# Optimization experiments

Measured on AMD Instinct MI355X. Metric: run time of the kernel, lower is better.

## Reference

```python
import jax, jax.numpy as jnp
import numpy as np

N_NODES = 100000
N_EDGES = 1600000
D_FEAT = 128
HIDDEN = 256
N_CLASSES = 40


def setup_inputs() -> dict:
    key = jax.random.key(0)
    ks = jax.random.split(key, 6)
    x = jax.random.normal(ks[0], (N_NODES, D_FEAT), dtype=jnp.float32)
    edge_index = jax.random.randint(ks[1], (2, N_EDGES), 0, N_NODES, dtype=jnp.int32)
    # Glorot-ish scaled weights
    w1_l = jax.random.normal(ks[2], (HIDDEN, D_FEAT), dtype=jnp.float32) / np.sqrt(D_FEAT)
    w1_r = jax.random.normal(ks[3], (HIDDEN, D_FEAT), dtype=jnp.float32) / np.sqrt(D_FEAT)
    w2_l = jax.random.normal(ks[4], (N_CLASSES, HIDDEN), dtype=jnp.float32) / np.sqrt(HIDDEN)
    w2_r = jax.random.normal(ks[5], (N_CLASSES, HIDDEN), dtype=jnp.float32) / np.sqrt(HIDDEN)
    b1_l = jnp.zeros((HIDDEN,), jnp.float32)
    b2_l = jnp.zeros((N_CLASSES,), jnp.float32)
    return {"x": x, "edge_index": edge_index, "w1_l": w1_l, "b1_l": b1_l,
            "w1_r": w1_r, "w2_l": w2_l, "b2_l": b2_l, "w2_r": w2_r}


def _sage_conv(x, src, dst, n_nodes, w_l, b_l, w_r):
    # mean aggregation of source-node features onto target nodes
    msg = x[src]                                                  # [E, d]
    agg = jax.ops.segment_sum(msg, dst, num_segments=n_nodes)     # [N, d]
    cnt = jax.ops.segment_sum(jnp.ones((dst.shape[0], 1), x.dtype), dst,
                              num_segments=n_nodes)               # [N, 1]
    agg = agg / jnp.maximum(cnt, 1.0)
    # out = lin_l(agg) + lin_r(x); lin_l has bias, lin_r does not (PyG default)
    return agg @ w_l.T + b_l + x @ w_r.T


def reference(x, edge_index, w1_l, b1_l, w1_r, w2_l, b2_l, w2_r):
    n_nodes = x.shape[0]
    src, dst = edge_index[0], edge_index[1]
    h = jax.nn.relu(_sage_conv(x, src, dst, n_nodes, w1_l, b1_l, w1_r))
    # dropout is identity in eval mode
    out = _sage_conv(h, src, dst, n_nodes, w2_l, b2_l, w2_r)
    return jax.nn.log_softmax(out, axis=1)
```

## Files before the change

### kernel.cpp

```cpp
#include <hip/hip_runtime.h>
#include <hip/hip_bf16.h>
#include <stdint.h>

#define NN 100000
#define NE 1600000
#define DF 128
#define DH 256
#define NC 40
#define BSHIFT 8
#define NBKT 391
#define EPB 8192
#define NBIN_BLOCKS ((NE + EPB - 1) / EPB)
#define BKT_SLACK 2048

typedef __attribute__((ext_vector_type(8))) short short8;
typedef __attribute__((ext_vector_type(4))) float f32x4;

typedef const __attribute__((address_space(1))) unsigned int* gas1;
typedef __attribute__((address_space(3))) unsigned int* las3;

__device__ __forceinline__ void gload16(const void* g, void* l) {
  __builtin_amdgcn_global_load_lds((gas1)g, (las3)l, 16, 0, 0);
}

__device__ __forceinline__ unsigned short f2bf(float f) {
  union { float f; unsigned u; } v; v.f = f;
  unsigned r = v.u + 0x7FFFu + ((v.u >> 16) & 1u);
  return (unsigned short)(r >> 16);
}
__device__ __forceinline__ float bflo(unsigned u) {
  union { unsigned u; float f; } v; v.u = u << 16; return v.f;
}
__device__ __forceinline__ float bfhi(unsigned u) {
  union { unsigned u; float f; } v; v.u = u & 0xFFFF0000u; return v.f;
}

__global__ void k_xbf16(const float* __restrict__ x, unsigned* __restrict__ xb) {
  int i = blockIdx.x * blockDim.x + threadIdx.x;
  if (i < (NN + 1) * 64) {
    unsigned pk = 0u;
    if (i < NN * 64) {
      float2 v = ((const float2*)x)[i];
      pk = ((unsigned)f2bf(v.y) << 16) | f2bf(v.x);
    }
    xb[i] = pk;
  }
}

__global__ __launch_bounds__(256) void k_bhist(const int* __restrict__ dst, int* __restrict__ bcnt) {
  __shared__ int h[NBKT];
  int tid = threadIdx.x;
  for (int b = tid; b < NBKT; b += 256) h[b] = 0;
  __syncthreads();
  int base = blockIdx.x * EPB;
  int n = NE - base; if (n > EPB) n = EPB;
  for (int i = tid; i < n; i += 256) atomicAdd(&h[dst[base + i] >> BSHIFT], 1);
  __syncthreads();
  for (int b = tid; b < NBKT; b += 256) if (h[b]) atomicAdd(&bcnt[b], h[b]);
}

__global__ __launch_bounds__(512) void k_bscan(const int* __restrict__ bcnt,
                                               int* __restrict__ boff, int* __restrict__ bcur,
                                               unsigned short* __restrict__ Pb) {
  __shared__ int s[512];
  int tid = threadIdx.x;
  int v = (tid < NBKT) ? bcnt[tid] : 0;
  s[tid] = v;
  __syncthreads();
  for (int off = 1; off < 512; off <<= 1) {
    int a = (tid >= off) ? s[tid - off] : 0;
    __syncthreads();
    s[tid] += a;
    __syncthreads();
  }
  int excl = s[tid] - v;
  if (tid < NBKT) { boff[tid] = excl; bcur[tid] = excl; }
  if (tid == NBKT) boff[NBKT] = excl;
  if (tid >= 448 && tid < 480) ((unsigned*)(Pb + (size_t)NN * 64))[tid - 448] = 0u;
}

__global__ __launch_bounds__(256) void k_bin(const int* __restrict__ src, const int* __restrict__ dst,
                                             int* __restrict__ bcur, unsigned* __restrict__ pairs) {
  __shared__ int hcnt[NBKT];
  __shared__ int hbase[NBKT];
  int tid = threadIdx.x;
  for (int b = tid; b < NBKT; b += 256) hcnt[b] = 0;
  __syncthreads();
  int base = blockIdx.x * EPB;
  int n = NE - base; if (n > EPB) n = EPB;
  for (int i = tid; i < n; i += 256) atomicAdd(&hcnt[dst[base + i] >> BSHIFT], 1);
  __syncthreads();
  for (int b = tid; b < NBKT; b += 256) hbase[b] = hcnt[b] ? atomicAdd(&bcur[b], hcnt[b]) : 0;
  __syncthreads();
  for (int b = tid; b < NBKT; b += 256) hcnt[b] = 0;
  __syncthreads();
  for (int i = tid; i < n; i += 256) {
    int s = src[base + i], d = dst[base + i];
    int b = d >> BSHIFT;
    int slot = atomicAdd(&hcnt[b], 1);
    pairs[hbase[b] + slot] = (unsigned)s | ((unsigned)(d & 255) << 17);
  }
}

__global__ __launch_bounds__(256) void k_csr(const unsigned* __restrict__ pairs,
                                             const int* __restrict__ boff,
                                             int* __restrict__ deg, int* __restrict__ row_ptr8,
                                             int* __restrict__ csr8) {
  __shared__ int ncnt[256];
  __shared__ int noff[256];
  int tid = threadIdx.x;
  int b = blockIdx.x;
  int base = boff[b], end = boff[b + 1];
  int base8 = base + BKT_SLACK * b;
  ncnt[tid] = 0;
  __syncthreads();
  for (int e = base + tid; e < end; e += 256) atomicAdd(&ncnt[pairs[e] >> 17], 1);
  __syncthreads();
  int cnt = ncnt[tid];
  int pcnt = (cnt + 7) & ~7;
  noff[tid] = pcnt;
  __syncthreads();
  for (int off = 1; off < 256; off <<= 1) {
    int a = (tid >= off) ? noff[tid - off] : 0;
    __syncthreads();
    noff[tid] += a;
    __syncthreads();
  }
  int pexcl = noff[tid] - pcnt;
  __syncthreads();
  noff[tid] = pexcl;
  ncnt[tid] = 0;
  __syncthreads();
  int gnode = (b << BSHIFT) + tid;
  if (gnode < NN) { deg[gnode] = cnt; row_ptr8[gnode] = base8 + pexcl; }
  for (int e = base + tid; e < end; e += 256) {
    unsigned p = pairs[e];
    int ld = p >> 17;
    int slot = atomicAdd(&ncnt[ld], 1);
    csr8[base8 + noff[ld] + slot] = (int)(p & 0x1FFFFu);
  }
  for (int k = cnt; k < pcnt; ++k) csr8[base8 + pexcl + k] = NN;
}

__global__ void k_packw(const float* __restrict__ w1l, const float* __restrict__ w1r,
                        const float* __restrict__ w2l, const float* __restrict__ w2r,
                        unsigned short* __restrict__ Wc, unsigned short* __restrict__ W2c) {
  int i = blockIdx.x * blockDim.x + threadIdx.x;
  if (i < 256 * 256) {
    int o = i >> 8, k = i & 255;
    float v = (k < 128) ? w1l[o * 128 + k] : w1r[o * 128 + (k - 128)];
    Wc[i] = f2bf(v);
  }
  int j = i - 256 * 256;
  if (j >= 0 && j < 80 * 256) {
    int o = j >> 8, k = j & 255;
    float v = (o < 40) ? w2l[o * 256 + k] : w2r[(o - 40) * 256 + k];
    W2c[j] = f2bf(v);
  }
}

__global__ void k_agg1(const unsigned* __restrict__ xb, const int* __restrict__ row_ptr8,
                       const int* __restrict__ deg, const int* __restrict__ csr8,
                       unsigned* __restrict__ A1) {
  int w = threadIdx.x >> 6, lane = threadIdx.x & 63;
  int node = blockIdx.x * 4 + w;
  if (node >= NN) return;
  int dg = deg[node];
  int rs = row_ptr8[node];
  int pdeg = (dg + 7) & ~7;
  int half = lane >> 5, li = lane & 31;
  float a0 = 0.f, a1 = 0.f, a2 = 0.f, a3 = 0.f;
  const unsigned* xp = xb + li * 2;
  for (int e = rs; e < rs + pdeg; e += 8) {
#pragma unroll
    for (int j = 0; j < 4; ++j) {
      int idx = csr8[e + 2 * j + half];
      uint2 v = *(const uint2*)(xp + (size_t)idx * 64);
      a0 += bflo(v.x); a1 += bfhi(v.x);
      a2 += bflo(v.y); a3 += bfhi(v.y);
    }
  }
  a0 += __shfl_xor(a0, 32);
  a1 += __shfl_xor(a1, 32);
  a2 += __shfl_xor(a2, 32);
  a3 += __shfl_xor(a3, 32);
  if (half == 0) {
    float inv = 1.f / (float)(dg > 0 ? dg : 1);
    uint2 pk;
    pk.x = ((unsigned)f2bf(a1 * inv) << 16) | f2bf(a0 * inv);
    pk.y = ((unsigned)f2bf(a3 * inv) << 16) | f2bf(a2 * inv);
    *(uint2*)(A1 + (size_t)node * 64 + li * 2) = pk;
  }
}

__global__ __launch_bounds__(256) void k_fused(const unsigned short* __restrict__ A1,
                                               const unsigned short* __restrict__ XB,
                                               const unsigned short* __restrict__ Wc,
                                               const float* __restrict__ b1,
                                               const unsigned short* __restrict__ W2c,
                                               unsigned short* __restrict__ Pb,
                                               float* __restrict__ R) {
  __shared__ __align__(16) unsigned short sA[64 * 64];
  __shared__ __align__(16) unsigned short sB[256 * 64];
  __shared__ __align__(16) unsigned short sH[64 * 256];
  int tid = threadIdx.x;
  int w = tid >> 6, lane = tid & 63;
  int brow = blockIdx.x * 64;
  int wr = (w >> 1) * 32, wc = (w & 1) * 128;
  f32x4 acc[2][8] = {};

  for (int kt = 0; kt < 4; ++kt) {
    const unsigned short* srcA = (kt < 2) ? A1 : XB;
    int kcol = (kt & 1) * 64;
#pragma unroll
    for (int t = 0; t < 2; ++t) {
      int c = t * 256 + tid;
      int r = c >> 3, cc = c & 7;
      int scc = cc ^ (r & 7);
      int gr = brow + r; if (gr > NN - 1) gr = NN - 1;
      gload16(srcA + (size_t)gr * 128 + kcol + scc * 8, sA + c * 8);
    }
#pragma unroll
    for (int t = 0; t < 8; ++t) {
      int c = t * 256 + tid;
      int r = c >> 3, cc = c & 7;
      int scc = cc ^ (r & 7);
      gload16(Wc + (size_t)r * 256 + kt * 64 + scc * 8, sB + c * 8);
    }
    __syncthreads();
#pragma unroll
    for (int kg = 0; kg < 2; ++kg) {
      short8 af[2], bfr[8];
#pragma unroll
      for (int m = 0; m < 2; ++m) {
        int row = wr + m * 16 + (lane & 15);
        int cch = (kg * 4 + (lane >> 4)) ^ (row & 7);
        af[m] = *(const short8*)(sA + row * 64 + cch * 8);
      }
#pragma unroll
      for (int n = 0; n < 8; ++n) {
        int row = wc + n * 16 + (lane & 15);
        int cch = (kg * 4 + (lane >> 4)) ^ (row & 7);
        bfr[n] = *(const short8*)(sB + row * 64 + cch * 8);
      }
#pragma unroll
      for (int m = 0; m < 2; ++m)
#pragma unroll
        for (int n = 0; n < 8; ++n)
          acc[m][n] = __builtin_amdgcn_mfma_f32_16x16x32_bf16(af[m], bfr[n], acc[m][n], 0, 0, 0);
    }
    __syncthreads();
  }

  {
    int colbase = wc + (lane & 15);
    int rowb = wr + (lane >> 4) * 4;
#pragma unroll
    for (int n = 0; n < 8; ++n) {
      int col = colbase + n * 16;
      float bias = b1[col];
      int g = col >> 3, off = col & 7;
#pragma unroll
      for (int m = 0; m < 2; ++m) {
        int row0 = rowb + m * 16;
#pragma unroll
        for (int q = 0; q < 4; ++q) {
          int row = row0 + q;
          float v = acc[m][n][q] + bias;
          v = v > 0.f ? v : 0.f;
          sH[row * 256 + ((g ^ (row & 7)) << 3) + off] = f2bf(v);
        }
      }
    }
  }
  __syncthreads();

  f32x4 a2[5] = {};
  int nrow = w * 16 + (lane & 15);
  for (int kt = 0; kt < 4; ++kt) {
#pragma unroll
    for (int t = 0; t < 3; ++t) {
      int c = t * 256 + tid;
      if (c < 640) {
        int r = c >> 3, cc = c & 7;
        int scc = cc ^ (r & 7);
        gload16(W2c + (size_t)r * 256 + kt * 64 + scc * 8, sB + c * 8);
      }
    }
    __syncthreads();
#pragma unroll
    for (int kg = 0; kg < 2; ++kg) {
      int gH = kt * 8 + kg * 4 + (lane >> 4);
      short8 bf1 = *(const short8*)(sH + nrow * 256 + ((gH ^ (nrow & 7)) << 3));
      short8 af[5];
#pragma unroll
      for (int m = 0; m < 5; ++m) {
        int arow = m * 16 + (lane & 15);
        int cch = (kg * 4 + (lane >> 4)) ^ (arow & 7);
        af[m] = *(const short8*)(sB + arow * 64 + cch * 8);
      }
#pragma unroll
      for (int m = 0; m < 5; ++m)
        a2[m] = __builtin_amdgcn_mfma_f32_16x16x32_bf16(af[m], bf1, a2[m], 0, 0, 0);
    }
    __syncthreads();
  }

  int node = brow + nrow;
  if (node < NN) {
#pragma unroll
    for (int m = 0; m < 5; ++m) {
      int c0 = m * 16 + (lane >> 4) * 4;
      f32x4 v = a2[m];
      if (c0 < NC) {
        uint2 pk;
        pk.x = ((unsigned)f2bf(v[1]) << 16) | f2bf(v[0]);
        pk.y = ((unsigned)f2bf(v[3]) << 16) | f2bf(v[2]);
        *(uint2*)(Pb + (size_t)node * 64 + c0) = pk;
      } else {
        if (c0 < 64) *(uint2*)(Pb + (size_t)node * 64 + c0) = make_uint2(0u, 0u);
        *(float4*)(R + (size_t)node * NC + (c0 - NC)) = make_float4(v[0], v[1], v[2], v[3]);
      }
    }
  }
}

__global__ __launch_bounds__(256) void k_final(const unsigned short* __restrict__ Pb,
                                               const float* __restrict__ R,
                                               const int* __restrict__ row_ptr8,
                                               const int* __restrict__ deg,
                                               const int* __restrict__ csr8,
                                               const float* __restrict__ b2,
                                               float* __restrict__ out) {
  int w = threadIdx.x >> 6, lane = threadIdx.x & 63;
  int g = lane >> 4, r = lane & 15;
  int node = blockIdx.x * 4 + w;
  if (node >= NN) return;
  int dg = deg[node];
  int rs = row_ptr8[node];
  int nfull = ((dg + 7) & ~7) >> 3;
  float s0 = 0.f, s1 = 0.f, s2 = 0.f, s3 = 0.f;
  int e = rs + g;
  for (int it = 0; it < nfull; ++it, e += 8) {
    int sa = csr8[e];
    int sb = csr8[e + 4];
    uint2 va = *(const uint2*)(Pb + (size_t)sa * 64 + r * 4);
    uint2 vb = *(const uint2*)(Pb + (size_t)sb * 64 + r * 4);
    s0 += bflo(va.x) + bflo(vb.x);
    s1 += bfhi(va.x) + bfhi(vb.x);
    s2 += bflo(va.y) + bflo(vb.y);
    s3 += bfhi(va.y) + bfhi(vb.y);
  }
  s0 += __shfl_xor(s0, 16); s0 += __shfl_xor(s0, 32);
  s1 += __shfl_xor(s1, 16); s1 += __shfl_xor(s1, 32);
  s2 += __shfl_xor(s2, 16); s2 += __shfl_xor(s2, 32);
  s3 += __shfl_xor(s3, 16); s3 += __shfl_xor(s3, 32);

  float inv = 1.f / (float)(dg > 0 ? dg : 1);
  bool act = r < 10;
  float4 rr = act ? *(const float4*)(R + (size_t)node * NC + r * 4) : make_float4(0, 0, 0, 0);
  float4 bb = act ? *(const float4*)(b2 + r * 4) : make_float4(0, 0, 0, 0);
  float v0 = s0 * inv + rr.x + bb.x;
  float v1 = s1 * inv + rr.y + bb.y;
  float v2 = s2 * inv + rr.z + bb.z;
  float v3 = s3 * inv + rr.w + bb.w;
  float mx = act ? fmaxf(fmaxf(v0, v1), fmaxf(v2, v3)) : -1e30f;
#pragma unroll
  for (int o = 1; o < 16; o <<= 1) mx = fmaxf(mx, __shfl_xor(mx, o));
  float ex = act ? (__expf(v0 - mx) + __expf(v1 - mx) + __expf(v2 - mx) + __expf(v3 - mx)) : 0.f;
#pragma unroll
  for (int o = 1; o < 16; o <<= 1) ex += __shfl_xor(ex, o);
  float ls = mx + __logf(ex);
  if (g == 0 && act) {
    float4 o4 = make_float4(v0 - ls, v1 - ls, v2 - ls, v3 - ls);
    *(float4*)(out + (size_t)node * NC + r * 4) = o4;
  }
}

extern "C" void kernel_launch(void* const* d_in, const int* in_sizes, int n_in,
                              void* d_out, int out_size, void* d_ws, size_t ws_size,
                              hipStream_t stream) {
  const float* x   = (const float*)d_in[0];
  const int*   ei  = (const int*)d_in[1];
  const float* w1l = (const float*)d_in[2];
  const float* b1  = (const float*)d_in[3];
  const float* w1r = (const float*)d_in[4];
  const float* w2l = (const float*)d_in[5];
  const float* b2  = (const float*)d_in[6];
  const float* w2r = (const float*)d_in[7];
  float* out = (float*)d_out;
  const int* src = ei;
  const int* dst = ei + NE;

  char* ws = (char*)d_ws;
  size_t off = 0;
  auto alloc = [&](size_t bytes) -> char* {
    char* p = ws + off;
    off = (off + bytes + 255) & ~(size_t)255;
    return p;
  };
  int* bcnt     = (int*)alloc((size_t)(NBKT + 1) * 4);
  int* boff     = (int*)alloc((size_t)(NBKT + 1) * 4);
  int* bcur     = (int*)alloc((size_t)NBKT * 4);
  int* deg      = (int*)alloc((size_t)NN * 4);
  int* row_ptr8 = (int*)alloc((size_t)NN * 4);
  unsigned* pairs = (unsigned*)alloc((size_t)NE * 4);
  int* csr8     = (int*)alloc((size_t)(NE + BKT_SLACK * NBKT + 64) * 4);
  unsigned short* Wc  = (unsigned short*)alloc(256 * 256 * 2);
  unsigned short* W2c = (unsigned short*)alloc(80 * 256 * 2);
  unsigned*       xb  = (unsigned*)alloc((size_t)(NN + 1) * 64 * 4);
  unsigned*       A1  = (unsigned*)alloc((size_t)NN * 64 * 4);
  unsigned short* Pb  = (unsigned short*)alloc((size_t)(NN + 1) * 64 * 2);
  float*          R   = (float*)alloc((size_t)NN * NC * 4);

  hipMemsetAsync(bcnt, 0, (size_t)(NBKT + 1) * 4, stream);
  k_bhist<<<NBIN_BLOCKS, 256, 0, stream>>>(dst, bcnt);
  k_xbf16<<<((NN + 1) * 64 + 255) / 256, 256, 0, stream>>>(x, xb);
  k_bscan<<<1, 512, 0, stream>>>(bcnt, boff, bcur, Pb);
  k_bin<<<NBIN_BLOCKS, 256, 0, stream>>>(src, dst, bcur, pairs);
  k_csr<<<NBKT, 256, 0, stream>>>(pairs, boff, deg, row_ptr8, csr8);
  k_packw<<<336, 256, 0, stream>>>(w1l, w1r, w2l, w2r, Wc, W2c);
  k_agg1<<<(NN + 3) / 4, 256, 0, stream>>>(xb, row_ptr8, deg, csr8, A1);
  k_fused<<<(NN + 63) / 64, 256, 0, stream>>>((const unsigned short*)A1,
                                              (const unsigned short*)xb, Wc, b1, W2c, Pb, R);
  k_final<<<(NN + 3) / 4, 256, 0, stream>>>(Pb, R, row_ptr8, deg, csr8, b2, out);
}
```

Baseline: 328.0 us.

## Vectorize bf16 conversion and enlarge block sizes for binning, CSR and final kernels

The x-to-bf16 conversion now has each thread read 8 floats and write a 16-byte packed vector, replacing one float2 per thread. The histogram and bin kernels go to 512 threads, the CSR build to 1024 threads (only 256 of them do the per-node scan work), and the final aggregation to 8 nodes per 512-thread block. The aim is wider memory transactions and more threads on the atomic-heavy preprocessing. In exchange, the 1024-thread CSR blocks leave most threads idle through the scan and add predicated branches. A pack2 helper is also factored out.

```diff
diff --git a/kernel.cpp b/kernel.cpp
--- a/kernel.cpp
+++ b/kernel.cpp
@@ -28,6 +28,9 @@
   unsigned r = v.u + 0x7FFFu + ((v.u >> 16) & 1u);
   return (unsigned short)(r >> 16);
 }
+__device__ __forceinline__ unsigned pack2(float a, float b) {
+  return ((unsigned)f2bf(b) << 16) | f2bf(a);
+}
 __device__ __forceinline__ float bflo(unsigned u) {
   union { unsigned u; float f; } v; v.u = u << 16; return v.f;
 }
@@ -37,26 +40,28 @@
 
 __global__ void k_xbf16(const float* __restrict__ x, unsigned* __restrict__ xb) {
   int i = blockIdx.x * blockDim.x + threadIdx.x;
-  if (i < (NN + 1) * 64) {
-    unsigned pk = 0u;
-    if (i < NN * 64) {
-      float2 v = ((const float2*)x)[i];
-      pk = ((unsigned)f2bf(v.y) << 16) | f2bf(v.x);
-    }
-    xb[i] = pk;
-  }
-}
-
-__global__ __launch_bounds__(256) void k_bhist(const int* __restrict__ dst, int* __restrict__ bcnt) {
+  if (i < (NN + 1) * 16) {
+    uint4 o = make_uint4(0u, 0u, 0u, 0u);
+    if (i < NN * 16) {
+      float4 a = ((const float4*)x)[2 * i];
+      float4 b = ((const float4*)x)[2 * i + 1];
+      o.x = pack2(a.x, a.y); o.y = pack2(a.z, a.w);
+      o.z = pack2(b.x, b.y); o.w = pack2(b.z, b.w);
+    }
+    ((uint4*)xb)[i] = o;
+  }
+}
+
+__global__ __launch_bounds__(512) void k_bhist(const int* __restrict__ dst, int* __restrict__ bcnt) {
   __shared__ int h[NBKT];
   int tid = threadIdx.x;
-  for (int b = tid; b < NBKT; b += 256) h[b] = 0;
+  for (int b = tid; b < NBKT; b += 512) h[b] = 0;
   __syncthreads();
   int base = blockIdx.x * EPB;
   int n = NE - base; if (n > EPB) n = EPB;
-  for (int i = tid; i < n; i += 256) atomicAdd(&h[dst[base + i] >> BSHIFT], 1);
-  __syncthreads();
-  for (int b = tid; b < NBKT; b += 256) if (h[b]) atomicAdd(&bcnt[b], h[b]);
+  for (int i = tid; i < n; i += 512) atomicAdd(&h[dst[base + i] >> BSHIFT], 1);
+  __syncthreads();
+  for (int b = tid; b < NBKT; b += 512) if (h[b]) atomicAdd(&bcnt[b], h[b]);
 }
 
 __global__ __launch_bounds__(512) void k_bscan(const int* __restrict__ bcnt,
@@ -79,22 +84,22 @@
   if (tid >= 448 && tid < 480) ((unsigned*)(Pb + (size_t)NN * 64))[tid - 448] = 0u;
 }
 
-__global__ __launch_bounds__(256) void k_bin(const int* __restrict__ src, const int* __restrict__ dst,
+__global__ __launch_bounds__(512) void k_bin(const int* __restrict__ src, const int* __restrict__ dst,
                                              int* __restrict__ bcur, unsigned* __restrict__ pairs) {
   __shared__ int hcnt[NBKT];
   __shared__ int hbase[NBKT];
   int tid = threadIdx.x;
-  for (int b = tid; b < NBKT; b += 256) hcnt[b] = 0;
+  for (int b = tid; b < NBKT; b += 512) hcnt[b] = 0;
   __syncthreads();
   int base = blockIdx.x * EPB;
   int n = NE - base; if (n > EPB) n = EPB;
-  for (int i = tid; i < n; i += 256) atomicAdd(&hcnt[dst[base + i] >> BSHIFT], 1);
-  __syncthreads();
-  for (int b = tid; b < NBKT; b += 256) hbase[b] = hcnt[b] ? atomicAdd(&bcur[b], hcnt[b]) : 0;
-  __syncthreads();
-  for (int b = tid; b < NBKT; b += 256) hcnt[b] = 0;
-  __syncthreads();
-  for (int i = tid; i < n; i += 256) {
+  for (int i = tid; i < n; i += 512) atomicAdd(&hcnt[dst[base + i] >> BSHIFT], 1);
+  __syncthreads();
+  for (int b = tid; b < NBKT; b += 512) hbase[b] = hcnt[b] ? atomicAdd(&bcur[b], hcnt[b]) : 0;
+  __syncthreads();
+  for (int b = tid; b < NBKT; b += 512) hcnt[b] = 0;
+  __syncthreads();
+  for (int i = tid; i < n; i += 512) {
     int s = src[base + i], d = dst[base + i];
     int b = d >> BSHIFT;
     int slot = atomicAdd(&hcnt[b], 1);
@@ -102,44 +107,48 @@
   }
 }
 
-__global__ __launch_bounds__(256) void k_csr(const unsigned* __restrict__ pairs,
-                                             const int* __restrict__ boff,
-                                             int* __restrict__ deg, int* __restrict__ row_ptr8,
-                                             int* __restrict__ csr8) {
+__global__ __launch_bounds__(1024) void k_csr(const unsigned* __restrict__ pairs,
+                                              const int* __restrict__ boff,
+                                              int* __restrict__ deg, int* __restrict__ row_ptr8,
+                                              int* __restrict__ csr8) {
   __shared__ int ncnt[256];
   __shared__ int noff[256];
   int tid = threadIdx.x;
   int b = blockIdx.x;
   int base = boff[b], end = boff[b + 1];
   int base8 = base + BKT_SLACK * b;
-  ncnt[tid] = 0;
-  __syncthreads();
-  for (int e = base + tid; e < end; e += 256) atomicAdd(&ncnt[pairs[e] >> 17], 1);
-  __syncthreads();
-  int cnt = ncnt[tid];
-  int pcnt = (cnt + 7) & ~7;
-  noff[tid] = pcnt;
+  if (tid < 256) ncnt[tid] = 0;
+  __syncthreads();
+  for (int e = base + tid; e < end; e += 1024) atomicAdd(&ncnt[pairs[e] >> 17], 1);
+  __syncthreads();
+  int cnt = 0, pcnt = 0;
+  if (tid < 256) { cnt = ncnt[tid]; pcnt = (cnt + 7) & ~7; noff[tid] = pcnt; }
   __syncthreads();
   for (int off = 1; off < 256; off <<= 1) {
-    int a = (tid >= off) ? noff[tid - off] : 0;
-    __syncthreads();
-    noff[tid] += a;
-    __syncthreads();
-  }
-  int pexcl = noff[tid] - pcnt;
-  __syncthreads();
-  noff[tid] = pexcl;
-  ncnt[tid] = 0;
-  __syncthreads();
-  int gnode = (b << BSHIFT) + tid;
-  if (gnode < NN) { deg[gnode] = cnt; row_ptr8[gnode] = base8 + pexcl; }
-  for (int e = base + tid; e < end; e += 256) {
+    int a = 0;
+    if (tid < 256 && tid >= off) a = noff[tid - off];
+    __syncthreads();
+    if (tid < 256) noff[tid] += a;
+    __syncthreads();
+  }
+  int pexcl = 0;
+  if (tid < 256) pexcl = noff[tid] - pcnt;
+  __syncthreads();
+  if (tid < 256) { noff[tid] = pexcl; ncnt[tid] = 0; }
+  __syncthreads();
+  if (tid < 256) {
+    int gnode = (b << BSHIFT) + tid;
+    if (gnode < NN) { deg[gnode] = cnt; row_ptr8[gnode] = base8 + pexcl; }
+  }
+  for (int e = base + tid; e < end; e += 1024) {
     unsigned p = pairs[e];
     int ld = p >> 17;
     int slot = atomicAdd(&ncnt[ld], 1);
     csr8[base8 + noff[ld] + slot] = (int)(p & 0x1FFFFu);
   }
-  for (int k = cnt; k < pcnt; ++k) csr8[base8 + pexcl + k] = NN;
+  if (tid < 256) {
+    for (int k = cnt; k < pcnt; ++k) csr8[base8 + pexcl + k] = NN;
+  }
 }
 
 __global__ void k_packw(const float* __restrict__ w1l, const float* __restrict__ w1r,
@@ -187,8 +196,8 @@
   if (half == 0) {
     float inv = 1.f / (float)(dg > 0 ? dg : 1);
     uint2 pk;
-    pk.x = ((unsigned)f2bf(a1 * inv) << 16) | f2bf(a0 * inv);
-    pk.y = ((unsigned)f2bf(a3 * inv) << 16) | f2bf(a2 * inv);
+    pk.x = pack2(a0 * inv, a1 * inv);
+    pk.y = pack2(a2 * inv, a3 * inv);
     *(uint2*)(A1 + (size_t)node * 64 + li * 2) = pk;
   }
 }
@@ -314,8 +323,8 @@
       f32x4 v = a2[m];
       if (c0 < NC) {
         uint2 pk;
-        pk.x = ((unsigned)f2bf(v[1]) << 16) | f2bf(v[0]);
-        pk.y = ((unsigned)f2bf(v[3]) << 16) | f2bf(v[2]);
+        pk.x = pack2(v[0], v[1]);
+        pk.y = pack2(v[2], v[3]);
         *(uint2*)(Pb + (size_t)node * 64 + c0) = pk;
       } else {
         if (c0 < 64) *(uint2*)(Pb + (size_t)node * 64 + c0) = make_uint2(0u, 0u);
@@ -325,7 +334,7 @@
   }
 }
 
-__global__ __launch_bounds__(256) void k_final(const unsigned short* __restrict__ Pb,
+__global__ __launch_bounds__(512) void k_final(const unsigned short* __restrict__ Pb,
                                                const float* __restrict__ R,
                                                const int* __restrict__ row_ptr8,
                                                const int* __restrict__ deg,
@@ -334,7 +343,7 @@
                                                float* __restrict__ out) {
   int w = threadIdx.x >> 6, lane = threadIdx.x & 63;
   int g = lane >> 4, r = lane & 15;
-  int node = blockIdx.x * 4 + w;
+  int node = blockIdx.x * 8 + w;
   if (node >= NN) return;
   int dg = deg[node];
   int rs = row_ptr8[node];
@@ -414,14 +423,14 @@
   float*          R   = (float*)alloc((size_t)NN * NC * 4);
 
   hipMemsetAsync(bcnt, 0, (size_t)(NBKT + 1) * 4, stream);
-  k_bhist<<<NBIN_BLOCKS, 256, 0, stream>>>(dst, bcnt);
-  k_xbf16<<<((NN + 1) * 64 + 255) / 256, 256, 0, stream>>>(x, xb);
+  k_bhist<<<NBIN_BLOCKS, 512, 0, stream>>>(dst, bcnt);
+  k_xbf16<<<((NN + 1) * 16 + 255) / 256, 256, 0, stream>>>(x, xb);
   k_bscan<<<1, 512, 0, stream>>>(bcnt, boff, bcur, Pb);
-  k_bin<<<NBIN_BLOCKS, 256, 0, stream>>>(src, dst, bcur, pairs);
-  k_csr<<<NBKT, 256, 0, stream>>>(pairs, boff, deg, row_ptr8, csr8);
+  k_bin<<<NBIN_BLOCKS, 512, 0, stream>>>(src, dst, bcur, pairs);
+  k_csr<<<NBKT, 1024, 0, stream>>>(pairs, boff, deg, row_ptr8, csr8);
   k_packw<<<336, 256, 0, stream>>>(w1l, w1r, w2l, w2r, Wc, W2c);
   k_agg1<<<(NN + 3) / 4, 256, 0, stream>>>(xb, row_ptr8, deg, csr8, A1);
   k_fused<<<(NN + 63) / 64, 256, 0, stream>>>((const unsigned short*)A1,
                                               (const unsigned short*)xb, Wc, b1, W2c, Pb, R);
-  k_final<<<(NN + 3) / 4, 256, 0, stream>>>(Pb, R, row_ptr8, deg, csr8, b2, out);
-}
+  k_final<<<(NN + 7) / 8, 512, 0, stream>>>(Pb, R, row_ptr8, deg, csr8, b2, out);
+}
```

After: 308.2 us. 1.06x faster.
